# Kernel tuning notes

Hardware: AMD Instinct MI355X
Metric: run time of the kernel (lower is better)

## Reference

```python
import jax, jax.numpy as jnp
import numpy as np

B, N = 128, 512
D_MODEL = 512
N_EXPERTS = 8
N_ELEM = 4   # VALID_ELEMENTS = range(4)
N_CHG = 3    # VALID_CHARGES = range(-1, 2); stored as index 0..2


def setup_inputs() -> dict:
    key = jax.random.key(0)
    ks = jax.random.split(key, 9)
    s = 1.0 / np.sqrt(D_MODEL)  # torch nn.Linear default init bound
    X = jax.random.normal(ks[0], (B, N, D_MODEL), jnp.float32)
    E = jax.random.randint(ks[1], (B, N), 0, N_ELEM)          # element label per atom
    C = jax.random.randint(ks[2], (B, N), 0, N_CHG)           # charge-label index per atom
    Wg = jax.random.uniform(ks[3], (D_MODEL, N_EXPERTS), jnp.float32, -s, s)
    bg = jax.random.uniform(ks[4], (N_EXPERTS,), jnp.float32, -s, s)
    # per-expert, per-label scalar projections (the only weights reaching the output)
    We = jax.random.uniform(ks[5], (N_EXPERTS, N_ELEM, D_MODEL), jnp.float32, -s, s)
    be = jax.random.uniform(ks[6], (N_EXPERTS, N_ELEM), jnp.float32, -s, s)
    Wc = jax.random.uniform(ks[7], (N_EXPERTS, N_CHG, D_MODEL), jnp.float32, -s, s)
    bc = jax.random.uniform(ks[8], (N_EXPERTS, N_CHG), jnp.float32, -s, s)
    return {"X": X, "E": E, "C": C, "Wg": Wg, "bg": bg,
            "We": We, "be": be, "Wc": Wc, "bc": bc}


def reference(X, E, C, Wg, bg, We, be, Wc, bc):
    # Gating: softmax over experts per atom, summed over atoms -> [B, X]
    gate = jax.nn.softmax(X @ Wg + bg, axis=-1).sum(axis=1)

    # Label-routed scalar projections, computed for all labels then selected
    # (matches the source's compute-all-then-torch.where semantics; at selected
    # positions X_masked == X, so applying the linear to full X is identical).
    pe_all = jnp.einsum('bnd,xld->bnxl', X, We) + be          # [B,N,X,4]
    pc_all = jnp.einsum('bnd,xld->bnxl', X, Wc) + bc          # [B,N,X,3]
    pe = (pe_all * jax.nn.one_hot(E, N_ELEM, dtype=X.dtype)[:, :, None, :]).sum(-1)  # [B,N,X]
    pc = (pc_all * jax.nn.one_hot(C, N_CHG, dtype=X.dtype)[:, :, None, :]).sum(-1)   # [B,N,X]

    # per_atom_IE = pe * |pc|; expert returns -(per_atom_IE).sum over atoms
    expert_out = -(pe * jnp.abs(pc)).sum(axis=1)              # [B, X]
    return (gate * expert_out).sum(axis=-1)                   # [B]
```

## Files before the change

### kernel.cpp

```cpp
#include <hip/hip_runtime.h>


#define WPACK_OFF 0
#define BIAS_OFF  65536
#define G_OFF     66560
#define S_OFF     70656

typedef __bf16 bf16x8 __attribute__((ext_vector_type(8)));
typedef float  f32x4  __attribute__((ext_vector_type(4)));

__global__ __launch_bounds__(256) void prep_kernel(
    const float* __restrict__ Wg, const float* __restrict__ bg,
    const float* __restrict__ We, const float* __restrict__ be,
    const float* __restrict__ Wc, const float* __restrict__ bc,
    unsigned char* __restrict__ ws)
{
    int tid = blockIdx.x * 256 + threadIdx.x;
    __bf16* wpack = (__bf16*)(ws + WPACK_OFF);
    float*  bias  = (float*)(ws + BIAS_OFF);
    float*  gz    = (float*)(ws + G_OFF);

    if (tid < 32768) {
        int j    = tid & 7;
        int lane = (tid >> 3) & 63;
        int ni   = (tid >> 9) & 3;
        int kc   = tid >> 11;
        int col  = ni * 16 + (lane & 15);
        int k    = kc * 32 + (lane >> 4) * 8 + j;
        float v;
        if (col < 8)       v = Wg[k * 8 + col];
        else if (col < 40) v = We[(col - 8) * 512 + k];
        else               v = Wc[(col - 40) * 512 + k];
        wpack[tid] = (__bf16)v;
    } else if (tid < 32832) {
        int col = tid - 32768;
        float v;
        if (col < 8)       v = bg[col];
        else if (col < 40) v = be[col - 8];
        else               v = bc[col - 40];
        bias[col] = v;
    } else if (tid < 34880) {
        gz[tid - 32832] = 0.0f;
    }
}

__device__ inline bf16x8 load_conv(const float* __restrict__ p) {
    float4 u = *(const float4*)p;
    float4 v = *(const float4*)(p + 4);
    bf16x8 r;
    r[0] = (__bf16)u.x; r[1] = (__bf16)u.y; r[2] = (__bf16)u.z; r[3] = (__bf16)u.w;
    r[4] = (__bf16)v.x; r[5] = (__bf16)v.y; r[6] = (__bf16)v.z; r[7] = (__bf16)v.w;
    return r;
}

__global__ __launch_bounds__(256) void moe_main(
    const float* __restrict__ X, const int* __restrict__ E, const int* __restrict__ C,
    const unsigned char* __restrict__ ws,
    float* __restrict__ G, float* __restrict__ S)
{
    __shared__ float ylds[4][32 * 65];
    __shared__ float bias_s[64];

    const int tid  = threadIdx.x;
    const int wave = tid >> 6;
    const int lane = tid & 63;
    const int quad = lane >> 4;
    const int l16  = lane & 15;

    if (tid < 64) bias_s[tid] = *((const float*)(ws + BIAS_OFF) + tid);

    const int b     = blockIdx.x >> 2;
    const int atom0 = b * 512 + (blockIdx.x & 3) * 128 + wave * 32;

    const bf16x8* __restrict__ wp = (const bf16x8*)(ws + WPACK_OFF);

    const float* xr0 = X + (size_t)(atom0 + l16) * 512 + quad * 8;
    const float* xr1 = xr0 + 16 * 512;

    f32x4 acc[2][4];
    #pragma unroll
    for (int mi = 0; mi < 2; ++mi)
        #pragma unroll
        for (int ni = 0; ni < 4; ++ni)
            acc[mi][ni] = 0.0f;

    for (int kc = 0; kc < 16; ++kc) {
        bf16x8 a0 = load_conv(xr0 + kc * 32);
        bf16x8 a1 = load_conv(xr1 + kc * 32);
        const bf16x8* wpk = wp + kc * 256 + lane;
        bf16x8 b0 = wpk[0];
        bf16x8 b1 = wpk[64];
        bf16x8 b2 = wpk[128];
        bf16x8 b3 = wpk[192];
        acc[0][0] = __builtin_amdgcn_mfma_f32_16x16x32_bf16(a0, b0, acc[0][0], 0, 0, 0);
        acc[0][1] = __builtin_amdgcn_mfma_f32_16x16x32_bf16(a0, b1, acc[0][1], 0, 0, 0);
        acc[0][2] = __builtin_amdgcn_mfma_f32_16x16x32_bf16(a0, b2, acc[0][2], 0, 0, 0);
        acc[0][3] = __builtin_amdgcn_mfma_f32_16x16x32_bf16(a0, b3, acc[0][3], 0, 0, 0);
        acc[1][0] = __builtin_amdgcn_mfma_f32_16x16x32_bf16(a1, b0, acc[1][0], 0, 0, 0);
        acc[1][1] = __builtin_amdgcn_mfma_f32_16x16x32_bf16(a1, b1, acc[1][1], 0, 0, 0);
        acc[1][2] = __builtin_amdgcn_mfma_f32_16x16x32_bf16(a1, b2, acc[1][2], 0, 0, 0);
        acc[1][3] = __builtin_amdgcn_mfma_f32_16x16x32_bf16(a1, b3, acc[1][3], 0, 0, 0);
    }

    float* Y = ylds[wave];
    #pragma unroll
    for (int mi = 0; mi < 2; ++mi)
        #pragma unroll
        for (int ni = 0; ni < 4; ++ni)
            #pragma unroll
            for (int r = 0; r < 4; ++r) {
                int row = mi * 16 + quad * 4 + r;
                int col = ni * 16 + l16;
                Y[row * 65 + col] = acc[mi][ni][r];
            }
    __syncthreads();

    float Gv[8], Sv[8];
    #pragma unroll
    for (int x = 0; x < 8; ++x) { Gv[x] = 0.0f; Sv[x] = 0.0f; }

    if (lane < 32) {
        const int atom = atom0 + lane;
        const int e = E[atom];
        const int c = C[atom];
        const float* yr = Y + lane * 65;

        float lg[8], m = -1e30f;
        #pragma unroll
        for (int x = 0; x < 8; ++x) {
            lg[x] = yr[x] + bias_s[x];
            m = fmaxf(m, lg[x]);
        }
        float sum = 0.0f;
        #pragma unroll
        for (int x = 0; x < 8; ++x) {
            lg[x] = __expf(lg[x] - m);
            sum += lg[x];
        }
        float inv = 1.0f / sum;
        #pragma unroll
        for (int x = 0; x < 8; ++x) {
            Gv[x] = lg[x] * inv;
            float pe = yr[8 + x * 4 + e] + bias_s[8 + x * 4 + e];
            float pc = yr[40 + x * 3 + c] + bias_s[40 + x * 3 + c];
            Sv[x] = pe * fabsf(pc);
        }
    }

    #pragma unroll
    for (int x = 0; x < 8; ++x) {
        float g = Gv[x], s = Sv[x];
        for (int off = 32; off > 0; off >>= 1) {
            g += __shfl_down(g, off);
            s += __shfl_down(s, off);
        }
        if (lane == 0) {
            atomicAdd(&G[b * 8 + x], g);
            atomicAdd(&S[b * 8 + x], s);
        }
    }
}

__global__ void final_kernel(const unsigned char* __restrict__ ws,
                             float* __restrict__ out)
{
    int b = threadIdx.x;
    const float* G = (const float*)(ws + G_OFF);
    const float* S = (const float*)(ws + S_OFF);
    if (b < 128) {
        float s = 0.0f;
        #pragma unroll
        for (int x = 0; x < 8; ++x) s += G[b * 8 + x] * S[b * 8 + x];
        out[b] = -s;
    }
}

extern "C" void kernel_launch(void* const* d_in, const int* in_sizes, int n_in,
                              void* d_out, int out_size, void* d_ws, size_t ws_size,
                              hipStream_t stream) {
    const float* X  = (const float*)d_in[0];
    const int*   E  = (const int*)d_in[1];
    const int*   C  = (const int*)d_in[2];
    const float* Wg = (const float*)d_in[3];
    const float* bg = (const float*)d_in[4];
    const float* We = (const float*)d_in[5];
    const float* be = (const float*)d_in[6];
    const float* Wc = (const float*)d_in[7];
    const float* bc = (const float*)d_in[8];
    unsigned char* ws = (unsigned char*)d_ws;
    float* out = (float*)d_out;

    float* G = (float*)(ws + G_OFF);
    float* S = (float*)(ws + S_OFF);

    hipLaunchKernelGGL(prep_kernel, dim3(137), dim3(256), 0, stream,
                       Wg, bg, We, be, Wc, bc, ws);
    hipLaunchKernelGGL(moe_main, dim3(512), dim3(256), 0, stream,
                       X, E, C, ws, G, S);
    hipLaunchKernelGGL(final_kernel, dim3(1), dim3(128), 0, stream, ws, out);
}
```

Before: 211.4 us.

## Halve per-wave atom tile, double grid, prefetch X, and aggregate atomics in LDS

Each wave now handles 16 atoms instead of 32, so the grid grows from 512 to 1024 blocks, raising occupancy and the number of memory requests in flight for the bandwidth-bound X read. The K loop software-prefetches the next X chunk before issuing the MFMAs. Per-block reductions go through shared-memory atomics first, so each block issues a single global atomic per expert. Each weight fragment is now reused across half as many atoms, which doubles weight loads from L2 per atom.

Measured after the change: 213.5 us. No clear change (+1.0%).

```diff
diff --git a/kernel.cpp b/kernel.cpp
--- a/kernel.cpp
+++ b/kernel.cpp
@@ -58,8 +58,9 @@
     const unsigned char* __restrict__ ws,
     float* __restrict__ G, float* __restrict__ S)
 {
-    __shared__ float ylds[4][32 * 65];
+    __shared__ float ylds[4][16 * 65];
     __shared__ float bias_s[64];
+    __shared__ float gacc[8], sacc[8];
 
     const int tid  = threadIdx.x;
     const int wave = tid >> 6;
@@ -68,58 +69,49 @@
     const int l16  = lane & 15;
 
     if (tid < 64) bias_s[tid] = *((const float*)(ws + BIAS_OFF) + tid);
+    if (tid < 8) { gacc[tid] = 0.0f; sacc[tid] = 0.0f; }
 
-    const int b     = blockIdx.x >> 2;
-    const int atom0 = b * 512 + (blockIdx.x & 3) * 128 + wave * 32;
+    const int atom0 = blockIdx.x * 64 + wave * 16;
+    const int b     = blockIdx.x >> 3;
 
     const bf16x8* __restrict__ wp = (const bf16x8*)(ws + WPACK_OFF);
 
-    const float* xr0 = X + (size_t)(atom0 + l16) * 512 + quad * 8;
-    const float* xr1 = xr0 + 16 * 512;
+    const float* xr = X + (size_t)(atom0 + l16) * 512 + quad * 8;
 
-    f32x4 acc[2][4];
+    f32x4 acc[4];
     #pragma unroll
-    for (int mi = 0; mi < 2; ++mi)
-        #pragma unroll
-        for (int ni = 0; ni < 4; ++ni)
-            acc[mi][ni] = 0.0f;
+    for (int ni = 0; ni < 4; ++ni) acc[ni] = 0.0f;
 
+    bf16x8 a = load_conv(xr);
+    #pragma unroll 2
     for (int kc = 0; kc < 16; ++kc) {
-        bf16x8 a0 = load_conv(xr0 + kc * 32);
-        bf16x8 a1 = load_conv(xr1 + kc * 32);
         const bf16x8* wpk = wp + kc * 256 + lane;
         bf16x8 b0 = wpk[0];
         bf16x8 b1 = wpk[64];
         bf16x8 b2 = wpk[128];
         bf16x8 b3 = wpk[192];
-        acc[0][0] = __builtin_amdgcn_mfma_f32_16x16x32_bf16(a0, b0, acc[0][0], 0, 0, 0);
-        acc[0][1] = __builtin_amdgcn_mfma_f32_16x16x32_bf16(a0, b1, acc[0][1], 0, 0, 0);
-        acc[0][2] = __builtin_amdgcn_mfma_f32_16x16x32_bf16(a0, b2, acc[0][2], 0, 0, 0);
-        acc[0][3] = __builtin_amdgcn_mfma_f32_16x16x32_bf16(a0, b3, acc[0][3], 0, 0, 0);
-        acc[1][0] = __builtin_amdgcn_mfma_f32_16x16x32_bf16(a1, b0, acc[1][0], 0, 0, 0);
-        acc[1][1] = __builtin_amdgcn_mfma_f32_16x16x32_bf16(a1, b1, acc[1][1], 0, 0, 0);
-        acc[1][2] = __builtin_amdgcn_mfma_f32_16x16x32_bf16(a1, b2, acc[1][2], 0, 0, 0);
-        acc[1][3] = __builtin_amdgcn_mfma_f32_16x16x32_bf16(a1, b3, acc[1][3], 0, 0, 0);
+        bf16x8 an = a;
+        if (kc < 15) an = load_conv(xr + (kc + 1) * 32);
+        acc[0] = __builtin_amdgcn_mfma_f32_16x16x32_bf16(a, b0, acc[0], 0, 0, 0);
+        acc[1] = __builtin_amdgcn_mfma_f32_16x16x32_bf16(a, b1, acc[1], 0, 0, 0);
+        acc[2] = __builtin_amdgcn_mfma_f32_16x16x32_bf16(a, b2, acc[2], 0, 0, 0);
+        acc[3] = __builtin_amdgcn_mfma_f32_16x16x32_bf16(a, b3, acc[3], 0, 0, 0);
+        a = an;
     }
 
     float* Y = ylds[wave];
     #pragma unroll
-    for (int mi = 0; mi < 2; ++mi)
+    for (int ni = 0; ni < 4; ++ni)
         #pragma unroll
-        for (int ni = 0; ni < 4; ++ni)
-            #pragma unroll
-            for (int r = 0; r < 4; ++r) {
-                int row = mi * 16 + quad * 4 + r;
-                int col = ni * 16 + l16;
-                Y[row * 65 + col] = acc[mi][ni][r];
-            }
+        for (int r = 0; r < 4; ++r)
+            Y[(quad * 4 + r) * 65 + ni * 16 + l16] = acc[ni][r];
     __syncthreads();
 
     float Gv[8], Sv[8];
     #pragma unroll
     for (int x = 0; x < 8; ++x) { Gv[x] = 0.0f; Sv[x] = 0.0f; }
 
-    if (lane < 32) {
+    if (lane < 16) {
         const int atom = atom0 + lane;
         const int e = E[atom];
         const int c = C[atom];
@@ -150,14 +142,20 @@
     #pragma unroll
     for (int x = 0; x < 8; ++x) {
         float g = Gv[x], s = Sv[x];
-        for (int off = 32; off > 0; off >>= 1) {
+        #pragma unroll
+        for (int off = 8; off > 0; off >>= 1) {
             g += __shfl_down(g, off);
             s += __shfl_down(s, off);
         }
         if (lane == 0) {
-            atomicAdd(&G[b * 8 + x], g);
-            atomicAdd(&S[b * 8 + x], s);
+            atomicAdd(&gacc[x], g);
+            atomicAdd(&sacc[x], s);
         }
+    }
+    __syncthreads();
+    if (tid < 8) {
+        atomicAdd(&G[b * 8 + tid], gacc[tid]);
+        atomicAdd(&S[b * 8 + tid], sacc[tid]);
     }
 }
 
@@ -195,7 +193,7 @@
 
     hipLaunchKernelGGL(prep_kernel, dim3(137), dim3(256), 0, stream,
                        Wg, bg, We, be, Wc, bc, ws);
-    hipLaunchKernelGGL(moe_main, dim3(512), dim3(256), 0, stream,
+    hipLaunchKernelGGL(moe_main, dim3(1024), dim3(256), 0, stream,
                        X, E, C, ws, G, S);
     hipLaunchKernelGGL(final_kernel, dim3(1), dim3(128), 0, stream, ws, out);
 }
```
